# Kernel optimization log

Hardware: AMD Instinct MI355X
Metric: run time of the kernel (lower is better)

## Reference

```python
import jax, jax.numpy as jnp
import numpy as np

VOL_RANGE = jnp.array([-20.0, -20.0, -2.0, 20.0, 20.0, 4.4], dtype=jnp.float32)
VOXEL_SIZE = 0.5
GRID_SHAPE = (80, 80, 12)  # int((max-min)/voxel_size) per axis, matching torch .int() truncation
OPACITY_THRESH = 1e-4
N_GAUSSIANS = 512
FEAT_DIM = 32


def _grid_flat():
    # Voxel-center coordinates, flattened to [V, 3] (V = 80*80*12 = 76800)
    coords = [jnp.arange(s, dtype=jnp.float32) + 0.5 for s in GRID_SHAPE]
    g = jnp.stack(jnp.meshgrid(*coords, indexing='ij'), axis=-1)
    g = g * VOXEL_SIZE + VOL_RANGE[:3]
    return g.reshape(-1, 3)


def _quat_to_rotmat(q):
    q = q / jnp.linalg.norm(q, axis=-1, keepdims=True)
    w, x, y, z = q[:, 0], q[:, 1], q[:, 2], q[:, 3]
    r0 = jnp.stack([1 - 2 * (y * y + z * z), 2 * (x * y - w * z), 2 * (x * z + w * y)], axis=-1)
    r1 = jnp.stack([2 * (x * y + w * z), 1 - 2 * (x * x + z * z), 2 * (y * z - w * x)], axis=-1)
    r2 = jnp.stack([2 * (x * z - w * y), 2 * (y * z + w * x), 1 - 2 * (x * x + y * y)], axis=-1)
    return jnp.stack([r0, r1, r2], axis=1)  # [N, 3, 3]


def setup_inputs() -> dict:
    key = jax.random.key(0)
    k1, k2, k3, k4, k5 = jax.random.split(key, 5)
    N, F = N_GAUSSIANS, FEAT_DIM
    vol_min = VOL_RANGE[:3]
    vol_max = VOL_RANGE[3:]
    # Sample means slightly beyond the volume so the bounds filter is exercised
    means3d = vol_min - 2.0 + jax.random.uniform(k1, (N, 3), dtype=jnp.float32) * (vol_max - vol_min + 4.0)
    opacities = jax.random.uniform(k2, (N, 1), dtype=jnp.float32)
    # SPD covariances: R diag(sigma^2) R^T with sigma in [0.2, 1.0] m
    R = _quat_to_rotmat(jax.random.normal(k3, (N, 4), dtype=jnp.float32))
    sigma = 0.2 + 0.8 * jax.random.uniform(k4, (N, 3), dtype=jnp.float32)
    covariances = jnp.einsum('nij,nj,nkj->nik', R, sigma ** 2, R)
    features = jax.random.normal(k5, (N, F), dtype=jnp.float32)
    return {"means3d": means3d, "opacities": opacities, "covariances": covariances, "features": features}


def reference(means3d, opacities, covariances, features):
    grid_flat = _grid_flat()  # [V, 3]
    vmin, vmax = VOL_RANGE[:3], VOL_RANGE[3:]

    # --- _filter_gaussians, expressed as a zero-opacity mask (math-equivalent to compaction) ---
    sigma = jnp.sqrt(jnp.diagonal(covariances, axis1=1, axis2=2))  # [N, 3]
    bmin = means3d - 3.0 * sigma
    bmax = means3d + 3.0 * sigma
    opac = opacities[:, 0]
    keep = jnp.all(bmax > vmin, axis=1) & jnp.all(bmin < vmax, axis=1) & (opac > OPACITY_THRESH)
    opac = opac * keep.astype(opac.dtype)

    # --- Mahalanobis splat (dense equivalent of the chunked loop) ---
    cov_inv = jnp.linalg.inv(covariances)  # [N, 3, 3]
    diff = means3d[:, None, :] - grid_flat[None, :, :]  # [N, V, 3]
    maha = jnp.einsum('nvi,nij,nvj->nv', diff, cov_inv, diff)  # [N, V]
    sigma_max = sigma.max(axis=1)  # [N]
    dist_sq = jnp.sum(diff * diff, axis=-1)  # [N, V]
    within = dist_sq < (3.0 * sigma_max[:, None]) ** 2
    contrib = opac[:, None] * jnp.exp(-0.5 * maha) * within.astype(maha.dtype)  # [N, V]

    density = contrib.sum(axis=0).reshape(*GRID_SHAPE, 1)
    grid_feats = jnp.einsum('nv,nf->vf', contrib, features).reshape(*GRID_SHAPE, features.shape[-1])
    grid_feats = grid_feats / jnp.maximum(density, 1e-6)
    return density, grid_feats
```

## Files before the change

### kernel.cpp

```cpp
#include <hip/hip_runtime.h>
#include <math.h>

#define NG 512
#define NV 76800
#define FD 32
#define CAP 160

__global__ __launch_bounds__(768) void voxelize_kernel(
    const float* __restrict__ means, const float* __restrict__ opac,
    const float* __restrict__ cov, const float* __restrict__ feats,
    float* __restrict__ out)
{
    __shared__ float4 gp[CAP];
    __shared__ float4 gq[CAP];
    __shared__ float4 gt[CAP];
    __shared__ float  gf[CAP][FD];
    __shared__ int    s_n[CAP];
    __shared__ int    s_cnt;

    const int tid  = threadIdx.x;
    const int lane = tid & 63;

    const int b   = blockIdx.x;
    const int tiy = b % 10;
    const int tix = b / 10;

    const float xlo = (tix * 8 + 0.5f) * 0.5f - 20.f, xhi = xlo + 3.5f;
    const float ylo = (tiy * 8 + 0.5f) * 0.5f - 20.f, yhi = ylo + 3.5f;
    const float zlo = 0.5f * 0.5f - 2.f,               zhi = zlo + 5.5f;

    if (tid == 0) s_cnt = 0;
    __syncthreads();

    if (tid < NG) {
        const int n = tid;
        const float a = cov[n*9+0], bb = cov[n*9+1], c = cov[n*9+2];
        const float d = cov[n*9+4], e  = cov[n*9+5], f = cov[n*9+8];
        const float sx = sqrtf(a), sy = sqrtf(d), sz = sqrtf(f);
        const float mx = means[n*3+0], my = means[n*3+1], mz = means[n*3+2];
        const float op = opac[n];
        const bool keep =
            (mx + 3.f*sx > -20.f) && (my + 3.f*sy > -20.f) && (mz + 3.f*sz > -2.f) &&
            (mx - 3.f*sx <  20.f) && (my - 3.f*sy <  20.f) && (mz - 3.f*sz <  4.4f) &&
            (op > 1e-4f);
        const float smax = fmaxf(sx, fmaxf(sy, sz));
        const float r2 = 9.f * smax * smax;
        const float cx = fminf(fmaxf(mx, xlo), xhi) - mx;
        const float cy = fminf(fmaxf(my, ylo), yhi) - my;
        const float cz = fminf(fmaxf(mz, zlo), zhi) - mz;
        const float d2t = cx*cx + cy*cy + cz*cz;
        const bool pred = keep && (d2t < r2);

        const unsigned long long m = __ballot(pred);
        int wofs = 0;
        if (lane == 0) wofs = atomicAdd(&s_cnt, (int)__popcll(m));
        wofs = __shfl(wofs, 0);
        const int pos = wofs + (int)__popcll(m & ((1ull << lane) - 1ull));
        if (pred && pos < CAP) {
            const float det = a*(d*f - e*e) - bb*(bb*f - c*e) + c*(bb*e - c*d);
            const float id = 1.f / det;
            gp[pos] = make_float4(mx, my, mz, r2);
            gq[pos] = make_float4((d*f - e*e) * id,
                                  (c*e - bb*f) * id,
                                  (bb*e - c*d) * id,
                                  (a*f - c*c) * id);
            gt[pos] = make_float4((bb*c - a*e) * id,
                                  (a*d - bb*bb) * id,
                                  op, 0.f);
            s_n[pos] = n;
        }
    }
    __syncthreads();
    const int ks = (s_cnt < CAP) ? s_cnt : CAP;

    for (int it = tid; it < ks * 8; it += 768) {
        const int s = it >> 3, j = it & 7;
        ((float4*)gf[s])[j] = ((const float4*)(feats + (size_t)s_n[s] * FD))[j];
    }
    __syncthreads();

    const int lz = tid % 12;
    const int lyx = tid / 12;
    const int ly = lyx % 8;
    const int lx = lyx / 8;
    const int ix = tix * 8 + lx;
    const int iy = tiy * 8 + ly;
    const int iz = lz;
    const float x = (ix + 0.5f) * 0.5f - 20.f;
    const float y = (iy + 0.5f) * 0.5f - 20.f;
    const float z = (iz + 0.5f) * 0.5f -  2.f;

    float dens = 0.f;
    float4 acc[8];
    #pragma unroll
    for (int j = 0; j < 8; ++j) acc[j] = make_float4(0.f, 0.f, 0.f, 0.f);

    for (int i = 0; i < ks; ++i) {
        const float4 p = gp[i];
        const float dx = p.x - x, dy = p.y - y, dz = p.z - z;
        const float d2 = dx*dx + dy*dy + dz*dz;
        if (d2 < p.w) {
            const float4 q = gq[i];
            const float4 t = gt[i];
            const float maha = q.x*dx*dx + q.w*dy*dy + t.y*dz*dz
                             + 2.f*(q.y*dx*dy + q.z*dx*dz + t.x*dy*dz);
            const float w = t.z * __expf(-0.5f * maha);
            dens += w;
            const float4* fp = (const float4*)gf[i];
            #pragma unroll
            for (int j = 0; j < 8; ++j) {
                const float4 f4 = fp[j];
                acc[j].x += w * f4.x; acc[j].y += w * f4.y;
                acc[j].z += w * f4.z; acc[j].w += w * f4.w;
            }
        }
    }

    const int v = (ix * 80 + iy) * 12 + iz;
    out[v] = dens;
    const float inv = 1.f / fmaxf(dens, 1e-6f);
    float4* fo = (float4*)(out + NV + (size_t)v * FD);
    #pragma unroll
    for (int j = 0; j < 8; ++j) {
        float4 rr;
        rr.x = acc[j].x * inv; rr.y = acc[j].y * inv;
        rr.z = acc[j].z * inv; rr.w = acc[j].w * inv;
        fo[j] = rr;
    }
}

extern "C" void kernel_launch(void* const* d_in, const int* in_sizes, int n_in,
                              void* d_out, int out_size, void* d_ws, size_t ws_size,
                              hipStream_t stream) {
    const float* means = (const float*)d_in[0];
    const float* opac  = (const float*)d_in[1];
    const float* cov   = (const float*)d_in[2];
    const float* feats = (const float*)d_in[3];
    float* out = (float*)d_out;
    voxelize_kernel<<<100, 768, 0, stream>>>(means, opac, cov, feats, out);
}
```

Measured before the change: 15.29 us.

## Split z into two tiles, split gaussian list across thread halves, prefetch branchlessly

The grid now uses 200 blocks, with each block covering half the z extent, so more CUs are busy. Within a block, two groups of 384 threads each take alternate gaussians and prefetch the next gaussian's parameters into registers. The data-dependent branch is replaced by a predicated weight, and partial sums are reduced through shared memory before the output is written. CAP drops from 160 to 64, which risks silently truncating gaussian lists for blocks with many overlapping gaussians. The branchless loop also does exp and feature FMAs for gaussians that fail the radius test.

```diff
diff --git a/kernel.cpp b/kernel.cpp
--- a/kernel.cpp
+++ b/kernel.cpp
@@ -4,30 +4,33 @@
 #define NG 512
 #define NV 76800
 #define FD 32
-#define CAP 160
+#define CAP 64
 
-__global__ __launch_bounds__(768) void voxelize_kernel(
+__global__ __launch_bounds__(768, 3) void voxelize_kernel(
     const float* __restrict__ means, const float* __restrict__ opac,
     const float* __restrict__ cov, const float* __restrict__ feats,
     float* __restrict__ out)
 {
-    __shared__ float4 gp[CAP];
-    __shared__ float4 gq[CAP];
-    __shared__ float4 gt[CAP];
-    __shared__ float  gf[CAP][FD];
-    __shared__ int    s_n[CAP];
-    __shared__ int    s_cnt;
+    __shared__ float pool[33 * 384];
+    __shared__ int   s_n[CAP];
+    __shared__ int   s_cnt;
+
+    float4* gp = (float4*)pool;
+    float4* gq = gp + (CAP + 4);
+    float4* gt = gq + (CAP + 4);
+    float*  gf = (float*)(gt + (CAP + 4));
 
     const int tid  = threadIdx.x;
     const int lane = tid & 63;
 
     const int b   = blockIdx.x;
-    const int tiy = b % 10;
-    const int tix = b / 10;
+    const int tiz = b % 2;
+    const int tiy = (b / 2) % 10;
+    const int tix = b / 20;
 
     const float xlo = (tix * 8 + 0.5f) * 0.5f - 20.f, xhi = xlo + 3.5f;
     const float ylo = (tiy * 8 + 0.5f) * 0.5f - 20.f, yhi = ylo + 3.5f;
-    const float zlo = 0.5f * 0.5f - 2.f,               zhi = zlo + 5.5f;
+    const float zlo = (tiz * 6 + 0.5f) * 0.5f -  2.f, zhi = zlo + 2.5f;
 
     if (tid == 0) s_cnt = 0;
     __syncthreads();
@@ -73,19 +76,27 @@
     __syncthreads();
     const int ks = (s_cnt < CAP) ? s_cnt : CAP;
 
+    if (tid < 4) {
+        gp[ks + tid] = make_float4(1e9f, 1e9f, 1e9f, -1.f);
+        gq[ks + tid] = make_float4(0.f, 0.f, 0.f, 0.f);
+        gt[ks + tid] = make_float4(0.f, 0.f, 0.f, 0.f);
+    }
+    if (tid < 32) ((float4*)(gf + ks * FD))[tid] = make_float4(0.f, 0.f, 0.f, 0.f);
+
     for (int it = tid; it < ks * 8; it += 768) {
         const int s = it >> 3, j = it & 7;
-        ((float4*)gf[s])[j] = ((const float4*)(feats + (size_t)s_n[s] * FD))[j];
+        ((float4*)(gf + s * FD))[j] = ((const float4*)(feats + (size_t)s_n[s] * FD))[j];
     }
     __syncthreads();
 
-    const int lz = tid % 12;
-    const int lyx = tid / 12;
-    const int ly = lyx % 8;
-    const int lx = lyx / 8;
+    const int sl = tid / 384;
+    const int u  = tid - sl * 384;
+    const int lz = u % 6;
+    const int ly = (u / 6) % 8;
+    const int lx = u / 48;
     const int ix = tix * 8 + lx;
     const int iy = tiy * 8 + ly;
-    const int iz = lz;
+    const int iz = tiz * 6 + lz;
     const float x = (ix + 0.5f) * 0.5f - 20.f;
     const float y = (iy + 0.5f) * 0.5f - 20.f;
     const float z = (iz + 0.5f) * 0.5f -  2.f;
@@ -95,37 +106,67 @@
     #pragma unroll
     for (int j = 0; j < 8; ++j) acc[j] = make_float4(0.f, 0.f, 0.f, 0.f);
 
-    for (int i = 0; i < ks; ++i) {
-        const float4 p = gp[i];
+    float4 p = gp[sl], q = gq[sl], t = gt[sl];
+    float4 f[8];
+    #pragma unroll
+    for (int j = 0; j < 8; ++j) f[j] = ((float4*)(gf + sl * FD))[j];
+
+    for (int i = sl; i < ks; i += 2) {
+        const int ip = i + 2;
+        const float4 pn = gp[ip], qn = gq[ip], tn = gt[ip];
+        float4 fn[8];
+        #pragma unroll
+        for (int j = 0; j < 8; ++j) fn[j] = ((float4*)(gf + ip * FD))[j];
+
         const float dx = p.x - x, dy = p.y - y, dz = p.z - z;
         const float d2 = dx*dx + dy*dy + dz*dz;
-        if (d2 < p.w) {
-            const float4 q = gq[i];
-            const float4 t = gt[i];
-            const float maha = q.x*dx*dx + q.w*dy*dy + t.y*dz*dz
-                             + 2.f*(q.y*dx*dy + q.z*dx*dz + t.x*dy*dz);
-            const float w = t.z * __expf(-0.5f * maha);
-            dens += w;
-            const float4* fp = (const float4*)gf[i];
-            #pragma unroll
-            for (int j = 0; j < 8; ++j) {
-                const float4 f4 = fp[j];
-                acc[j].x += w * f4.x; acc[j].y += w * f4.y;
-                acc[j].z += w * f4.z; acc[j].w += w * f4.w;
-            }
+        const float maha = q.x*dx*dx + q.w*dy*dy + t.y*dz*dz
+                         + 2.f*(q.y*dx*dy + q.z*dx*dz + t.x*dy*dz);
+        float w = t.z * __expf(-0.5f * maha);
+        w = (d2 < p.w) ? w : 0.f;
+        dens += w;
+        #pragma unroll
+        for (int j = 0; j < 8; ++j) {
+            acc[j].x += w * f[j].x; acc[j].y += w * f[j].y;
+            acc[j].z += w * f[j].z; acc[j].w += w * f[j].w;
+        }
+        p = pn; q = qn; t = tn;
+        #pragma unroll
+        for (int j = 0; j < 8; ++j) f[j] = fn[j];
+    }
+
+    __syncthreads();
+    if (sl == 1) {
+        pool[u] = dens;
+        #pragma unroll
+        for (int j = 0; j < 8; ++j) {
+            pool[(1 + j*4 + 0) * 384 + u] = acc[j].x;
+            pool[(1 + j*4 + 1) * 384 + u] = acc[j].y;
+            pool[(1 + j*4 + 2) * 384 + u] = acc[j].z;
+            pool[(1 + j*4 + 3) * 384 + u] = acc[j].w;
         }
     }
-
-    const int v = (ix * 80 + iy) * 12 + iz;
-    out[v] = dens;
-    const float inv = 1.f / fmaxf(dens, 1e-6f);
-    float4* fo = (float4*)(out + NV + (size_t)v * FD);
-    #pragma unroll
-    for (int j = 0; j < 8; ++j) {
-        float4 rr;
-        rr.x = acc[j].x * inv; rr.y = acc[j].y * inv;
-        rr.z = acc[j].z * inv; rr.w = acc[j].w * inv;
-        fo[j] = rr;
+    __syncthreads();
+    if (sl == 0) {
+        dens += pool[u];
+        #pragma unroll
+        for (int j = 0; j < 8; ++j) {
+            acc[j].x += pool[(1 + j*4 + 0) * 384 + u];
+            acc[j].y += pool[(1 + j*4 + 1) * 384 + u];
+            acc[j].z += pool[(1 + j*4 + 2) * 384 + u];
+            acc[j].w += pool[(1 + j*4 + 3) * 384 + u];
+        }
+        const int v = (ix * 80 + iy) * 12 + iz;
+        out[v] = dens;
+        const float inv = 1.f / fmaxf(dens, 1e-6f);
+        float4* fo = (float4*)(out + NV + (size_t)v * FD);
+        #pragma unroll
+        for (int j = 0; j < 8; ++j) {
+            float4 rr;
+            rr.x = acc[j].x * inv; rr.y = acc[j].y * inv;
+            rr.z = acc[j].z * inv; rr.w = acc[j].w * inv;
+            fo[j] = rr;
+        }
     }
 }
 
@@ -137,5 +178,5 @@
     const float* cov   = (const float*)d_in[2];
     const float* feats = (const float*)d_in[3];
     float* out = (float*)d_out;
-    voxelize_kernel<<<100, 768, 0, stream>>>(means, opac, cov, feats, out);
+    voxelize_kernel<<<200, 768, 0, stream>>>(means, opac, cov, feats, out);
 }
```

Measured after the change: 13.92 us. 9.0% less time.

## Retile into smaller 10x10x3 voxel blocks with bitmask culling and direct feature reads

Applied to the files above, without the earlier changes.

Splits the volume into 256 blocks of 10x10x3 voxels (320 threads, 300 active) instead of 100 blocks of 8x8x12, so more CUs are used and each tile culls more Gaussians. Each thread first builds a 64-bit hit mask over the candidate list, then visits only the set bits. Features are now read straight from global memory (cached) rather than staged in LDS. The per-tile capacity drops from 160 to 64, which silently truncates if a tile has more than 64 candidates. Reading features from global memory may also add load latency.

```diff
diff --git a/kernel.cpp b/kernel.cpp
--- a/kernel.cpp
+++ b/kernel.cpp
@@ -4,9 +4,9 @@
 #define NG 512
 #define NV 76800
 #define FD 32
-#define CAP 160
+#define CAP 64
 
-__global__ __launch_bounds__(768) void voxelize_kernel(
+__global__ __launch_bounds__(320) void voxelize_kernel(
     const float* __restrict__ means, const float* __restrict__ opac,
     const float* __restrict__ cov, const float* __restrict__ feats,
     float* __restrict__ out)
@@ -14,7 +14,6 @@
     __shared__ float4 gp[CAP];
     __shared__ float4 gq[CAP];
     __shared__ float4 gt[CAP];
-    __shared__ float  gf[CAP][FD];
     __shared__ int    s_n[CAP];
     __shared__ int    s_cnt;
 
@@ -22,91 +21,98 @@
     const int lane = tid & 63;
 
     const int b   = blockIdx.x;
-    const int tiy = b % 10;
-    const int tix = b / 10;
+    const int tiz = b & 3;
+    const int tiy = (b >> 2) & 7;
+    const int tix = b >> 5;
 
-    const float xlo = (tix * 8 + 0.5f) * 0.5f - 20.f, xhi = xlo + 3.5f;
-    const float ylo = (tiy * 8 + 0.5f) * 0.5f - 20.f, yhi = ylo + 3.5f;
-    const float zlo = 0.5f * 0.5f - 2.f,               zhi = zlo + 5.5f;
+    const float xlo = (tix * 10 + 0.5f) * 0.5f - 20.f, xhi = xlo + 4.5f;
+    const float ylo = (tiy * 10 + 0.5f) * 0.5f - 20.f, yhi = ylo + 4.5f;
+    const float zlo = (tiz * 3  + 0.5f) * 0.5f -  2.f, zhi = zlo + 1.0f;
 
     if (tid == 0) s_cnt = 0;
     __syncthreads();
 
-    if (tid < NG) {
-        const int n = tid;
-        const float a = cov[n*9+0], bb = cov[n*9+1], c = cov[n*9+2];
-        const float d = cov[n*9+4], e  = cov[n*9+5], f = cov[n*9+8];
-        const float sx = sqrtf(a), sy = sqrtf(d), sz = sqrtf(f);
-        const float mx = means[n*3+0], my = means[n*3+1], mz = means[n*3+2];
-        const float op = opac[n];
-        const bool keep =
-            (mx + 3.f*sx > -20.f) && (my + 3.f*sy > -20.f) && (mz + 3.f*sz > -2.f) &&
-            (mx - 3.f*sx <  20.f) && (my - 3.f*sy <  20.f) && (mz - 3.f*sz <  4.4f) &&
-            (op > 1e-4f);
-        const float smax = fmaxf(sx, fmaxf(sy, sz));
-        const float r2 = 9.f * smax * smax;
-        const float cx = fminf(fmaxf(mx, xlo), xhi) - mx;
-        const float cy = fminf(fmaxf(my, ylo), yhi) - my;
-        const float cz = fminf(fmaxf(mz, zlo), zhi) - mz;
-        const float d2t = cx*cx + cy*cy + cz*cz;
-        const bool pred = keep && (d2t < r2);
+    #pragma unroll
+    for (int r = 0; r < 2; ++r) {
+        const int n = r * 320 + tid;
+        if (n < NG) {
+            const float a = cov[n*9+0], bb = cov[n*9+1], c = cov[n*9+2];
+            const float d = cov[n*9+4], e  = cov[n*9+5], f = cov[n*9+8];
+            const float sx = sqrtf(a), sy = sqrtf(d), sz = sqrtf(f);
+            const float mx = means[n*3+0], my = means[n*3+1], mz = means[n*3+2];
+            const float op = opac[n];
+            const bool keep =
+                (mx + 3.f*sx > -20.f) && (my + 3.f*sy > -20.f) && (mz + 3.f*sz > -2.f) &&
+                (mx - 3.f*sx <  20.f) && (my - 3.f*sy <  20.f) && (mz - 3.f*sz <  4.4f) &&
+                (op > 1e-4f);
+            const float smax = fmaxf(sx, fmaxf(sy, sz));
+            const float r2 = 9.f * smax * smax;
+            const float cx = fminf(fmaxf(mx, xlo), xhi) - mx;
+            const float cy = fminf(fmaxf(my, ylo), yhi) - my;
+            const float cz = fminf(fmaxf(mz, zlo), zhi) - mz;
+            const float d2t = cx*cx + cy*cy + cz*cz;
+            const bool pred = keep && (d2t < r2);
 
-        const unsigned long long m = __ballot(pred);
-        int wofs = 0;
-        if (lane == 0) wofs = atomicAdd(&s_cnt, (int)__popcll(m));
-        wofs = __shfl(wofs, 0);
-        const int pos = wofs + (int)__popcll(m & ((1ull << lane) - 1ull));
-        if (pred && pos < CAP) {
-            const float det = a*(d*f - e*e) - bb*(bb*f - c*e) + c*(bb*e - c*d);
-            const float id = 1.f / det;
-            gp[pos] = make_float4(mx, my, mz, r2);
-            gq[pos] = make_float4((d*f - e*e) * id,
-                                  (c*e - bb*f) * id,
-                                  (bb*e - c*d) * id,
-                                  (a*f - c*c) * id);
-            gt[pos] = make_float4((bb*c - a*e) * id,
-                                  (a*d - bb*bb) * id,
-                                  op, 0.f);
-            s_n[pos] = n;
+            const unsigned long long m = __ballot(pred);
+            int wofs = 0;
+            if (lane == 0) wofs = atomicAdd(&s_cnt, (int)__popcll(m));
+            wofs = __shfl(wofs, 0);
+            const int pos = wofs + (int)__popcll(m & ((1ull << lane) - 1ull));
+            if (pred && pos < CAP) {
+                const float det = a*(d*f - e*e) - bb*(bb*f - c*e) + c*(bb*e - c*d);
+                const float id = 1.f / det;
+                gp[pos] = make_float4(mx, my, mz, r2);
+                gq[pos] = make_float4((d*f - e*e) * id,
+                                      (c*e - bb*f) * id,
+                                      (bb*e - c*d) * id,
+                                      (a*f - c*c) * id);
+                gt[pos] = make_float4((bb*c - a*e) * id,
+                                      (a*d - bb*bb) * id,
+                                      op, 0.f);
+                s_n[pos] = n;
+            }
         }
     }
     __syncthreads();
     const int ks = (s_cnt < CAP) ? s_cnt : CAP;
 
-    for (int it = tid; it < ks * 8; it += 768) {
-        const int s = it >> 3, j = it & 7;
-        ((float4*)gf[s])[j] = ((const float4*)(feats + (size_t)s_n[s] * FD))[j];
-    }
-    __syncthreads();
+    const int u = tid;
+    if (u < 300) {
+        const int lz = u % 3;
+        const int ly = (u / 3) % 10;
+        const int lx = u / 30;
+        const int ix = tix * 10 + lx;
+        const int iy = tiy * 10 + ly;
+        const int iz = tiz * 3  + lz;
+        const float x = (ix + 0.5f) * 0.5f - 20.f;
+        const float y = (iy + 0.5f) * 0.5f - 20.f;
+        const float z = (iz + 0.5f) * 0.5f -  2.f;
 
-    const int lz = tid % 12;
-    const int lyx = tid / 12;
-    const int ly = lyx % 8;
-    const int lx = lyx / 8;
-    const int ix = tix * 8 + lx;
-    const int iy = tiy * 8 + ly;
-    const int iz = lz;
-    const float x = (ix + 0.5f) * 0.5f - 20.f;
-    const float y = (iy + 0.5f) * 0.5f - 20.f;
-    const float z = (iz + 0.5f) * 0.5f -  2.f;
+        unsigned long long hm = 0ull;
+        for (int i = 0; i < ks; ++i) {
+            const float4 p = gp[i];
+            const float dx = p.x - x, dy = p.y - y, dz = p.z - z;
+            const float d2 = dx*dx + dy*dy + dz*dz;
+            hm |= (d2 < p.w) ? (1ull << i) : 0ull;
+        }
 
-    float dens = 0.f;
-    float4 acc[8];
-    #pragma unroll
-    for (int j = 0; j < 8; ++j) acc[j] = make_float4(0.f, 0.f, 0.f, 0.f);
+        float dens = 0.f;
+        float4 acc[8];
+        #pragma unroll
+        for (int j = 0; j < 8; ++j) acc[j] = make_float4(0.f, 0.f, 0.f, 0.f);
 
-    for (int i = 0; i < ks; ++i) {
-        const float4 p = gp[i];
-        const float dx = p.x - x, dy = p.y - y, dz = p.z - z;
-        const float d2 = dx*dx + dy*dy + dz*dz;
-        if (d2 < p.w) {
+        while (hm) {
+            const int i = (int)__builtin_ctzll(hm);
+            hm &= hm - 1ull;
+            const float4 p = gp[i];
             const float4 q = gq[i];
             const float4 t = gt[i];
+            const float dx = p.x - x, dy = p.y - y, dz = p.z - z;
             const float maha = q.x*dx*dx + q.w*dy*dy + t.y*dz*dz
                              + 2.f*(q.y*dx*dy + q.z*dx*dz + t.x*dy*dz);
             const float w = t.z * __expf(-0.5f * maha);
             dens += w;
-            const float4* fp = (const float4*)gf[i];
+            const float4* fp = (const float4*)(feats + (size_t)s_n[i] * FD);
             #pragma unroll
             for (int j = 0; j < 8; ++j) {
                 const float4 f4 = fp[j];
@@ -114,18 +120,18 @@
                 acc[j].z += w * f4.z; acc[j].w += w * f4.w;
             }
         }
-    }
 
-    const int v = (ix * 80 + iy) * 12 + iz;
-    out[v] = dens;
-    const float inv = 1.f / fmaxf(dens, 1e-6f);
-    float4* fo = (float4*)(out + NV + (size_t)v * FD);
-    #pragma unroll
-    for (int j = 0; j < 8; ++j) {
-        float4 rr;
-        rr.x = acc[j].x * inv; rr.y = acc[j].y * inv;
-        rr.z = acc[j].z * inv; rr.w = acc[j].w * inv;
-        fo[j] = rr;
+        const int v = (ix * 80 + iy) * 12 + iz;
+        out[v] = dens;
+        const float inv = 1.f / fmaxf(dens, 1e-6f);
+        float4* fo = (float4*)(out + NV + (size_t)v * FD);
+        #pragma unroll
+        for (int j = 0; j < 8; ++j) {
+            float4 rr;
+            rr.x = acc[j].x * inv; rr.y = acc[j].y * inv;
+            rr.z = acc[j].z * inv; rr.w = acc[j].w * inv;
+            fo[j] = rr;
+        }
     }
 }
 
@@ -137,5 +143,5 @@
     const float* cov   = (const float*)d_in[2];
     const float* feats = (const float*)d_in[3];
     float* out = (float*)d_out;
-    voxelize_kernel<<<100, 768, 0, stream>>>(means, opac, cov, feats, out);
+    voxelize_kernel<<<256, 320, 0, stream>>>(means, opac, cov, feats, out);
 }
```

Measured after the change: 14.06 us. 1.09x faster.

## Precompute per-voxel hit bitmasks, read features from global, stage output stores via LDS

Applied to the files above, without the earlier changes.

The kernel drops the shared-memory feature copy and now reads Gaussian features straight from global/L1. A first pass builds 64-bit hit masks per voxel, and the accumulation loop walks only the set bits instead of branching on every candidate. Output is staged through a double-buffered LDS tile, one x-slice at a time, so each slice is written with coalesced float4 stores. The staging adds 8 block-wide barriers. CAP drops from 160 to 128, which silently truncates blocks that have more overlapping Gaussians.

```diff
diff --git a/kernel.cpp b/kernel.cpp
--- a/kernel.cpp
+++ b/kernel.cpp
@@ -4,7 +4,7 @@
 #define NG 512
 #define NV 76800
 #define FD 32
-#define CAP 160
+#define CAP 128
 
 __global__ __launch_bounds__(768) void voxelize_kernel(
     const float* __restrict__ means, const float* __restrict__ opac,
@@ -14,9 +14,10 @@
     __shared__ float4 gp[CAP];
     __shared__ float4 gq[CAP];
     __shared__ float4 gt[CAP];
-    __shared__ float  gf[CAP][FD];
     __shared__ int    s_n[CAP];
     __shared__ int    s_cnt;
+    __shared__ float4 ldsF[2][96][9];
+    __shared__ float  ldsD[2][96];
 
     const int tid  = threadIdx.x;
     const int lane = tid & 63;
@@ -72,17 +73,12 @@
     }
     __syncthreads();
     const int ks = (s_cnt < CAP) ? s_cnt : CAP;
+    const int k0 = (ks < 64) ? ks : 64;
 
-    for (int it = tid; it < ks * 8; it += 768) {
-        const int s = it >> 3, j = it & 7;
-        ((float4*)gf[s])[j] = ((const float4*)(feats + (size_t)s_n[s] * FD))[j];
-    }
-    __syncthreads();
-
-    const int lz = tid % 12;
-    const int lyx = tid / 12;
-    const int ly = lyx % 8;
-    const int lx = lyx / 8;
+    const int lx  = tid / 96;
+    const int rem = tid - lx * 96;
+    const int ly  = rem / 12;
+    const int lz  = rem - ly * 12;
     const int ix = tix * 8 + lx;
     const int iy = tiy * 8 + ly;
     const int iz = lz;
@@ -90,23 +86,41 @@
     const float y = (iy + 0.5f) * 0.5f - 20.f;
     const float z = (iz + 0.5f) * 0.5f -  2.f;
 
+    unsigned long long hm0 = 0ull, hm1 = 0ull;
+    for (int i = 0; i < k0; ++i) {
+        const float4 p = gp[i];
+        const float dx = p.x - x, dy = p.y - y, dz = p.z - z;
+        const float d2 = dx*dx + dy*dy + dz*dz;
+        hm0 |= (d2 < p.w) ? (1ull << i) : 0ull;
+    }
+    for (int i = 64; i < ks; ++i) {
+        const float4 p = gp[i];
+        const float dx = p.x - x, dy = p.y - y, dz = p.z - z;
+        const float d2 = dx*dx + dy*dy + dz*dz;
+        hm1 |= (d2 < p.w) ? (1ull << (i - 64)) : 0ull;
+    }
+
     float dens = 0.f;
     float4 acc[8];
     #pragma unroll
     for (int j = 0; j < 8; ++j) acc[j] = make_float4(0.f, 0.f, 0.f, 0.f);
 
-    for (int i = 0; i < ks; ++i) {
-        const float4 p = gp[i];
-        const float dx = p.x - x, dy = p.y - y, dz = p.z - z;
-        const float d2 = dx*dx + dy*dy + dz*dz;
-        if (d2 < p.w) {
+    #pragma unroll
+    for (int wsel = 0; wsel < 2; ++wsel) {
+        unsigned long long hm = wsel ? hm1 : hm0;
+        const int ofs = wsel ? 64 : 0;
+        while (hm) {
+            const int i = (int)__builtin_ctzll(hm) + ofs;
+            hm &= hm - 1ull;
+            const float4 p = gp[i];
             const float4 q = gq[i];
             const float4 t = gt[i];
+            const float dx = p.x - x, dy = p.y - y, dz = p.z - z;
             const float maha = q.x*dx*dx + q.w*dy*dy + t.y*dz*dz
                              + 2.f*(q.y*dx*dy + q.z*dx*dz + t.x*dy*dz);
             const float w = t.z * __expf(-0.5f * maha);
             dens += w;
-            const float4* fp = (const float4*)gf[i];
+            const float4* fp = (const float4*)(feats + (size_t)s_n[i] * FD);
             #pragma unroll
             for (int j = 0; j < 8; ++j) {
                 const float4 f4 = fp[j];
@@ -116,16 +130,24 @@
         }
     }
 
-    const int v = (ix * 80 + iy) * 12 + iz;
-    out[v] = dens;
     const float inv = 1.f / fmaxf(dens, 1e-6f);
-    float4* fo = (float4*)(out + NV + (size_t)v * FD);
     #pragma unroll
     for (int j = 0; j < 8; ++j) {
-        float4 rr;
-        rr.x = acc[j].x * inv; rr.y = acc[j].y * inv;
-        rr.z = acc[j].z * inv; rr.w = acc[j].w * inv;
-        fo[j] = rr;
+        acc[j].x *= inv; acc[j].y *= inv; acc[j].z *= inv; acc[j].w *= inv;
+    }
+
+    for (int s = 0; s < 8; ++s) {
+        const int bi = s & 1;
+        if (lx == s) {
+            ldsD[bi][rem] = dens;
+            #pragma unroll
+            for (int j = 0; j < 8; ++j) ldsF[bi][rem][j] = acc[j];
+        }
+        __syncthreads();
+        const int Dbase = ((tix * 8 + s) * 80 + tiy * 8) * 12;
+        if (tid < 96) out[Dbase + tid] = ldsD[bi][tid];
+        const int vox = tid >> 3, j = tid & 7;
+        ((float4*)(out + NV + (size_t)Dbase * FD))[tid] = ldsF[bi][vox][j];
     }
 }
 
```

Result: slower. 15.88 us (+3.9%).
